# Performance work log

Measured on AMD Instinct MI355X. Metric: run time of the kernel, lower is better.

The kernel has to match this reference:

```python
import jax, jax.numpy as jnp
import numpy as np

MUL0, MUL1 = 64, 32          # 64x0e + 32x1e irreps_emb
D_FEAT = MUL0 + 3 * MUL1     # 160
N_T, N_Q, N_K = 64, 1024, 1024


def quat_apply(q, v):
    # q: (...,4) real-first (w,x,y,z); v: (...,3). Rotate v by q.
    w = q[..., :1]
    u = q[..., 1:]
    uv = jnp.cross(u, v)
    return v + 2.0 * (w * uv + jnp.cross(u, uv))


def split_irreps(f):
    # f: (..., 160) -> scalars (...,64), vectors (...,32,3)
    s = f[..., :MUL0]
    v = f[..., MUL0:].reshape(f.shape[:-1] + (MUL1, 3))
    return s, v


def dtp(a, b, Ws, Wv):
    # Depthwise tensor product restricted to l<=1 (SeparableFCTP analogue),
    # output irreps 1x0e + 32x1e, with SiLU activation on the scalar part.
    sa, va = split_irreps(a)
    sb, vb = split_irreps(b)
    # scalar paths: 0e*0e and 1e.1e (dot) -> 96 scalar channels
    scal = jnp.concatenate([sa * sb, jnp.einsum('...ci,...ci->...c', va, vb)], axis=-1)
    # vector paths: 0e*1e, 1e*0e, 1e x 1e (cross) -> 96 vector channels
    vec = jnp.concatenate(
        [sa[..., :MUL1, None] * vb, va * sb[..., :MUL1, None], jnp.cross(va, vb)], axis=-2)
    out_s = jax.nn.silu(scal @ Ws)                    # (...,1)
    out_v = jnp.einsum('...ci,co->...oi', vec, Wv)    # (...,32,3)
    return out_s, out_v


def get_key_features(points, key_coord, key_feat, W_key):
    # radius-style key lookup: nearest key node + smooth radial envelope + linear
    d2 = jnp.sum((points[:, None, :] - key_coord[None, :, :]) ** 2, axis=-1)  # (M, N_K)
    idx = jnp.argmin(d2, axis=-1)
    dist = jnp.sqrt(jnp.take_along_axis(d2, idx[:, None], axis=1)[:, 0])
    env = jnp.exp(-dist)[:, None]
    return (key_feat[idx] * env) @ W_key              # (M, 160)


def setup_inputs() -> dict:
    key = jax.random.key(0)
    ks = jax.random.split(key, 11)
    return {
        'T': jax.random.normal(ks[0], (N_T, 7), jnp.float32),
        'query_weight': jax.random.uniform(ks[1], (N_Q,), jnp.float32),
        'query_feature': jax.random.normal(ks[2], (N_Q, D_FEAT), jnp.float32),
        'query_coord': jax.random.normal(ks[3], (N_Q, 3), jnp.float32),
        'key_coord': jax.random.normal(ks[4], (N_K, 3), jnp.float32),
        'key_node_feature': jax.random.normal(ks[5], (N_K, D_FEAT), jnp.float32),
        'W_key': jax.random.normal(ks[6], (D_FEAT, D_FEAT), jnp.float32) / np.sqrt(D_FEAT),
        'Ws_lin': jax.random.normal(ks[7], (96, 1), jnp.float32) / np.sqrt(96.0),
        'Wv_lin': jax.random.normal(ks[8], (96, 32), jnp.float32) / np.sqrt(96.0),
        'Ws_ang': jax.random.normal(ks[9], (96, 1), jnp.float32) / np.sqrt(96.0),
        'Wv_ang': jax.random.normal(ks[10], (96, 32), jnp.float32) / np.sqrt(96.0),
    }


def reference(T, query_weight, query_feature, query_coord, key_coord,
              key_node_feature, W_key, Ws_lin, Wv_lin, Ws_ang, Wv_ang):
    n_t = T.shape[0]
    n_q = query_feature.shape[0]
    q = T[:, :4]
    q = q / jnp.linalg.norm(q, axis=-1, keepdims=True)
    X = T[:, 4:]
    # transform query coords by each pose: (N_T, N_Q, 3)
    qc_t = quat_apply(q[:, None, :], query_coord[None, :, :]) + X[:, None, :]
    # equivariant feature transform: scalars unchanged, vectors rotated
    s, v = split_irreps(query_feature)
    v_t = quat_apply(q[:, None, None, :], v[None])                    # (N_T,N_Q,32,3)
    qf_t = jnp.concatenate(
        [jnp.broadcast_to(s, (n_t,) + s.shape), v_t.reshape(n_t, n_q, 3 * MUL1)],
        axis=-1).reshape(n_t * n_q, D_FEAT)
    # key feature gather over the expanded N_T*N_Q batch
    kf = get_key_features(qc_t.reshape(-1, 3), key_coord, key_node_feature, W_key)
    # two tensor products; original drops leading scalar ([..., 1:])
    _, lin = dtp(qf_t, kf, Ws_lin, Wv_lin)
    _, ang = dtp(qf_t, kf, Ws_ang, Wv_ang)
    lin = lin.reshape(n_t, n_q, MUL1, 3).mean(axis=-2)
    ang = ang.reshape(n_t, n_q, MUL1, 3).mean(axis=-2)
    # rotate back into body frame
    qinv = q * jnp.array([1.0, -1.0, -1.0, -1.0], q.dtype)
    lin = quat_apply(qinv[:, None, :], lin)
    ang = quat_apply(qinv[:, None, :], ang)
    ang_orbital = jnp.cross(query_coord[None], lin)
    lin_vel = jnp.einsum('q,tqi->ti', query_weight, lin)
    ang_vel = jnp.einsum('q,tqi->ti', query_weight, ang_orbital + ang)
    return lin_vel, ang_vel
```

## Files before the change

kernel.cpp:

```cpp
#include <hip/hip_runtime.h>
#include <math.h>

#define NT 64
#define NQ 1024
#define NK 1024
#define WS_KW 0
#define WS_QF 131072
#define WS_WV 262144
#define WS_KP 262400

__launch_bounds__(256)
__global__ void prep_kernel(const float* __restrict__ qfeat,
                            const float* __restrict__ keyfeat,
                            const float* __restrict__ Wkey,
                            const float* __restrict__ WvL,
                            const float* __restrict__ WvA,
                            const float* __restrict__ kcoord,
                            float* __restrict__ ws,
                            float* __restrict__ out) {
  const int blk = blockIdx.x;
  const int tid = threadIdx.x;
  if (blk < 128) {
    const int g = blk * 256 + tid;
    const int r = g >> 5;
    const int c = g & 31;
    const float* kf = keyfeat + r * 160;
    const int c0 = 64 + 3 * c;
    float a0 = 0.f, a1 = 0.f, a2 = 0.f, a3 = 0.f;
#pragma unroll 4
    for (int k = 0; k < 160; ++k) {
      const float f = kf[k];
      const float* wr = Wkey + k * 160;
      a0 = fmaf(f, wr[c0 + 0], a0);
      a1 = fmaf(f, wr[c0 + 1], a1);
      a2 = fmaf(f, wr[c0 + 2], a2);
      a3 = fmaf(f, wr[c], a3);
    }
    reinterpret_cast<float4*>(ws + WS_KW)[g] = make_float4(a0, a1, a2, a3);
  } else if (blk < 256) {
    const int g = (blk - 128) * 256 + tid;
    const int p = g >> 5;
    const int c = g & 31;
    const float* q = qfeat + p * 160;
    float4 o = make_float4(q[64 + 3 * c], q[65 + 3 * c], q[66 + 3 * c], q[c]);
    reinterpret_cast<float4*>(ws + WS_QF)[c * 1024 + p] = o;
  } else {
    out[tid] = 0.f;
    if (tid < 128) out[256 + tid] = 0.f;
    float4* kp = reinterpret_cast<float4*>(ws + WS_KP);
#pragma unroll
    for (int j = 0; j < 4; ++j) {
      const int k = j * 256 + tid;
      kp[k] = make_float4(kcoord[k * 3 + 0], kcoord[k * 3 + 1], kcoord[k * 3 + 2], 0.f);
    }
    if (tid < 32) {
      const int c = tid;
      float m0 = 0.f, m1 = 0.f, m2 = 0.f, m3 = 0.f, m4 = 0.f, m5 = 0.f;
      for (int o = 0; o < 32; ++o) {
        m0 += WvL[c * 32 + o];
        m1 += WvL[(32 + c) * 32 + o];
        m2 += WvL[(64 + c) * 32 + o];
        m3 += WvA[c * 32 + o];
        m4 += WvA[(32 + c) * 32 + o];
        m5 += WvA[(64 + c) * 32 + o];
      }
      float* wv = ws + WS_WV + c * 8;
      const float s = 1.0f / 32.0f;
      wv[0] = m0 * s; wv[1] = m1 * s; wv[2] = m2 * s;
      wv[3] = m3 * s; wv[4] = m4 * s; wv[5] = m5 * s;
      wv[6] = 0.f; wv[7] = 0.f;
    }
  }
}

__launch_bounds__(512)
__global__ void main_kernel(const float* __restrict__ T,
                            const float* __restrict__ qweight,
                            const float* __restrict__ qcoord,
                            const float* __restrict__ ws,
                            float* __restrict__ out) {
  __shared__ float4 keys[1024];
  __shared__ float2 cand[8][256];
  __shared__ float red[8][8];
  const int tid  = threadIdx.x;
  const int lane = tid & 63;
  const int wu   = __builtin_amdgcn_readfirstlane(tid >> 6);
  const int t    = blockIdx.x >> 2;
  const int pg   = blockIdx.x & 3;

  {
    const float4* kp = reinterpret_cast<const float4*>(ws + WS_KP);
    keys[tid]       = kp[tid];
    keys[512 + tid] = kp[512 + tid];
  }

  const float* Tt = T + t * 7;
  float qw = Tt[0], qx = Tt[1], qy = Tt[2], qz = Tt[3];
  const float Xx = Tt[4], Xy = Tt[5], Xz = Tt[6];
  const float rn = rsqrtf(qw * qw + qx * qx + qy * qy + qz * qz);
  qw *= rn; qx *= rn; qy *= rn; qz *= rn;
  const float ix = -qx, iy = -qy, iz = -qz;

  float qcx[4], qcy[4], qcz[4];
#pragma unroll
  for (int j = 0; j < 4; ++j) {
    const int q = pg * 256 + j * 64 + lane;
    const float px = qcoord[q * 3 + 0];
    const float py = qcoord[q * 3 + 1];
    const float pz = qcoord[q * 3 + 2];
    const float ux = qy * pz - qz * py;
    const float uy = qz * px - qx * pz;
    const float uz = qx * py - qy * px;
    qcx[j] = px + 2.0f * (qw * ux + (qy * uz - qz * uy)) + Xx;
    qcy[j] = py + 2.0f * (qw * uy + (qz * ux - qx * uz)) + Xy;
    qcz[j] = pz + 2.0f * (qw * uz + (qx * uy - qy * ux)) + Xz;
  }

  __syncthreads();

  const int kbase = wu * 128;
  float mv0 = 1e30f, mv1 = 1e30f, mv2 = 1e30f, mv3 = 1e30f;
  int mi0 = 0, mi1 = 0, mi2 = 0, mi3 = 0;
#pragma unroll 4
  for (int m = 0; m < 128; ++m) {
    const float4 K = keys[kbase + m];
    const float d0x = qcx[0] - K.x, d0y = qcy[0] - K.y, d0z = qcz[0] - K.z;
    const float d1x = qcx[1] - K.x, d1y = qcy[1] - K.y, d1z = qcz[1] - K.z;
    const float d2x = qcx[2] - K.x, d2y = qcy[2] - K.y, d2z = qcz[2] - K.z;
    const float d3x = qcx[3] - K.x, d3y = qcy[3] - K.y, d3z = qcz[3] - K.z;
    const float d0 = d0x * d0x + d0y * d0y + d0z * d0z;
    const float d1 = d1x * d1x + d1y * d1y + d1z * d1z;
    const float d2 = d2x * d2x + d2y * d2y + d2z * d2z;
    const float d3 = d3x * d3x + d3y * d3y + d3z * d3z;
    const int ki = kbase + m;
    if (d0 < mv0) { mv0 = d0; mi0 = ki; }
    if (d1 < mv1) { mv1 = d1; mi1 = ki; }
    if (d2 < mv2) { mv2 = d2; mi2 = ki; }
    if (d3 < mv3) { mv3 = d3; mi3 = ki; }
  }
  cand[wu][0 * 64 + lane] = make_float2(mv0, __int_as_float(mi0));
  cand[wu][1 * 64 + lane] = make_float2(mv1, __int_as_float(mi1));
  cand[wu][2 * 64 + lane] = make_float2(mv2, __int_as_float(mi2));
  cand[wu][3 * 64 + lane] = make_float2(mv3, __int_as_float(mi3));
  __syncthreads();

  const int pl  = tid >> 1;
  const int sub = tid & 1;
  float mv; int mi;
  {
    const float2 c0 = cand[4 * sub][pl];
    mv = c0.x; mi = __float_as_int(c0.y);
#pragma unroll
    for (int i = 1; i < 4; ++i) {
      const float2 ci = cand[4 * sub + i][pl];
      const float vi = ci.x; const int ii = __float_as_int(ci.y);
      if (vi < mv || (vi == mv && ii < mi)) { mv = vi; mi = ii; }
    }
    const float vo = __shfl_xor(mv, 1);
    const int   io = __shfl_xor(mi, 1);
    if (vo < mv || (vo == mv && io < mi)) { mv = vo; mi = io; }
  }
  const int minidx = mi;
  const float env = expf(-sqrtf(mv));

  const int pF = pg * 256 + pl;
  const float qpx = qcoord[pF * 3 + 0];
  const float qpy = qcoord[pF * 3 + 1];
  const float qpz = qcoord[pF * 3 + 2];

  const float4* kwrow = reinterpret_cast<const float4*>(ws + WS_KW) + minidx * 32;
  const float4* qfp   = reinterpret_cast<const float4*>(ws + WS_QF) + pF;
  const float* wv = ws + WS_WV;
  float lx = 0.f, ly = 0.f, lz = 0.f, ax = 0.f, ay = 0.f, az = 0.f;
#pragma unroll
  for (int jj = 0; jj < 16; ++jj) {
    const int c = 2 * jj + sub;
    const float4 B = kwrow[c];
    const float4 A = qfp[c * 1024];
    const float uvx = iy * B.z - iz * B.y;
    const float uvy = iz * B.x - ix * B.z;
    const float uvz = ix * B.y - iy * B.x;
    const float bx = B.x + 2.0f * (qw * uvx + (iy * uvz - iz * uvy));
    const float by = B.y + 2.0f * (qw * uvy + (iz * uvx - ix * uvz));
    const float bz = B.z + 2.0f * (qw * uvz + (ix * uvy - iy * uvx));
    const float crx = A.y * bz - A.z * by;
    const float cry = A.z * bx - A.x * bz;
    const float crz = A.x * by - A.y * bx;
    const float* w6 = wv + c * 8;
    const float a1L = w6[0] * A.w, a2L = w6[1] * B.w, w3L = w6[2];
    const float a1A = w6[3] * A.w, a2A = w6[4] * B.w, w3A = w6[5];
    lx = fmaf(a1L, bx, fmaf(a2L, A.x, fmaf(w3L, crx, lx)));
    ly = fmaf(a1L, by, fmaf(a2L, A.y, fmaf(w3L, cry, ly)));
    lz = fmaf(a1L, bz, fmaf(a2L, A.z, fmaf(w3L, crz, lz)));
    ax = fmaf(a1A, bx, fmaf(a2A, A.x, fmaf(w3A, crx, ax)));
    ay = fmaf(a1A, by, fmaf(a2A, A.y, fmaf(w3A, cry, ay)));
    az = fmaf(a1A, bz, fmaf(a2A, A.z, fmaf(w3A, crz, az)));
  }
  lx += __shfl_xor(lx, 1); ly += __shfl_xor(ly, 1); lz += __shfl_xor(lz, 1);
  ax += __shfl_xor(ax, 1); ay += __shfl_xor(ay, 1); az += __shfl_xor(az, 1);
  lx *= env; ly *= env; lz *= env;
  ax *= env; ay *= env; az *= env;

  const float wp = qweight[pF];
  const float ox = qpy * lz - qpz * ly;
  const float oy = qpz * lx - qpx * lz;
  const float oz = qpx * ly - qpy * lx;
  float r0 = wp * lx, r1 = wp * ly, r2 = wp * lz;
  float r3 = wp * (ox + ax), r4 = wp * (oy + ay), r5 = wp * (oz + az);

#pragma unroll
  for (int m = 32; m >= 1; m >>= 1) {
    r0 += __shfl_xor(r0, m);
    r1 += __shfl_xor(r1, m);
    r2 += __shfl_xor(r2, m);
    r3 += __shfl_xor(r3, m);
    r4 += __shfl_xor(r4, m);
    r5 += __shfl_xor(r5, m);
  }
  if (lane == 0) {
    red[wu][0] = r0; red[wu][1] = r1; red[wu][2] = r2;
    red[wu][3] = r3; red[wu][4] = r4; red[wu][5] = r5;
  }
  __syncthreads();
  if (tid < 6) {
    float s = 0.f;
#pragma unroll
    for (int w = 0; w < 8; ++w) s += red[w][tid];
    const int row = (tid < 3) ? (t * 3 + tid) : (192 + t * 3 + (tid - 3));
    atomicAdd(out + row, s * 0.5f);
  }
}

extern "C" void kernel_launch(void* const* d_in, const int* in_sizes, int n_in,
                              void* d_out, int out_size, void* d_ws, size_t ws_size,
                              hipStream_t stream) {
  const float* T   = (const float*)d_in[0];
  const float* qw  = (const float*)d_in[1];
  const float* qf  = (const float*)d_in[2];
  const float* qc  = (const float*)d_in[3];
  const float* kc  = (const float*)d_in[4];
  const float* kf  = (const float*)d_in[5];
  const float* Wk  = (const float*)d_in[6];
  const float* WvL = (const float*)d_in[8];
  const float* WvA = (const float*)d_in[10];
  float* out = (float*)d_out;
  float* ws  = (float*)d_ws;

  prep_kernel<<<257, 256, 0, stream>>>(qf, kf, Wk, WvL, WvA, kc, ws, out);
  main_kernel<<<256, 512, 0, stream>>>(T, qw, qc, ws, out);
}
```

Before: 109.1 us.

## Repartition main kernel into 1024 blocks with 16-lane key split and shuffle argmin

The main kernel now launches 1024 blocks of 256 threads, each handling 64 queries for one transform. Each query's nearest-key search is split across 16 lanes with interleaved key indices, and the partial argmins are merged by xor-shuffles instead of a cross-wave shared-memory candidate reduction. The feature contraction now splits 4 ways per query instead of 2. This gives more blocks to fill the GPU's compute units and makes the argmin reduction cheaper. In exchange, every block reloads the full 1024-key table into LDS (four times as many blocks doing it) and issues four times as many output atomics.

New measurement: 108.8 us. Within noise of the previous version (-0.3%).

```diff
diff --git a/kernel.cpp b/kernel.cpp
--- a/kernel.cpp
+++ b/kernel.cpp
@@ -73,25 +73,26 @@
   }
 }
 
-__launch_bounds__(512)
+__launch_bounds__(256)
 __global__ void main_kernel(const float* __restrict__ T,
                             const float* __restrict__ qweight,
                             const float* __restrict__ qcoord,
                             const float* __restrict__ ws,
                             float* __restrict__ out) {
   __shared__ float4 keys[1024];
-  __shared__ float2 cand[8][256];
-  __shared__ float red[8][8];
+  __shared__ float2 cand[64];
+  __shared__ float red[4][8];
   const int tid  = threadIdx.x;
   const int lane = tid & 63;
-  const int wu   = __builtin_amdgcn_readfirstlane(tid >> 6);
-  const int t    = blockIdx.x >> 2;
-  const int pg   = blockIdx.x & 3;
+  const int t    = blockIdx.x >> 4;
+  const int qg   = blockIdx.x & 15;
+  const int sub  = tid & 15;
+  const int pl   = tid >> 4;
 
   {
     const float4* kp = reinterpret_cast<const float4*>(ws + WS_KP);
-    keys[tid]       = kp[tid];
-    keys[512 + tid] = kp[512 + tid];
+#pragma unroll
+    for (int j = 0; j < 4; ++j) keys[j * 256 + tid] = kp[j * 256 + tid];
   }
 
   const float* Tt = T + t * 7;
@@ -104,7 +105,7 @@
   float qcx[4], qcy[4], qcz[4];
 #pragma unroll
   for (int j = 0; j < 4; ++j) {
-    const int q = pg * 256 + j * 64 + lane;
+    const int q = qg * 64 + pl * 4 + j;
     const float px = qcoord[q * 3 + 0];
     const float py = qcoord[q * 3 + 1];
     const float pz = qcoord[q * 3 + 2];
@@ -118,12 +119,12 @@
 
   __syncthreads();
 
-  const int kbase = wu * 128;
   float mv0 = 1e30f, mv1 = 1e30f, mv2 = 1e30f, mv3 = 1e30f;
   int mi0 = 0, mi1 = 0, mi2 = 0, mi3 = 0;
-#pragma unroll 4
-  for (int m = 0; m < 128; ++m) {
-    const float4 K = keys[kbase + m];
+#pragma unroll 8
+  for (int m = 0; m < 64; ++m) {
+    const float4 K = keys[16 * m + sub];
+    const int ki = 16 * m + sub;
     const float d0x = qcx[0] - K.x, d0y = qcy[0] - K.y, d0z = qcz[0] - K.z;
     const float d1x = qcx[1] - K.x, d1y = qcy[1] - K.y, d1z = qcz[1] - K.z;
     const float d2x = qcx[2] - K.x, d2y = qcy[2] - K.y, d2z = qcz[2] - K.z;
@@ -132,38 +133,38 @@
     const float d1 = d1x * d1x + d1y * d1y + d1z * d1z;
     const float d2 = d2x * d2x + d2y * d2y + d2z * d2z;
     const float d3 = d3x * d3x + d3y * d3y + d3z * d3z;
-    const int ki = kbase + m;
     if (d0 < mv0) { mv0 = d0; mi0 = ki; }
     if (d1 < mv1) { mv1 = d1; mi1 = ki; }
     if (d2 < mv2) { mv2 = d2; mi2 = ki; }
     if (d3 < mv3) { mv3 = d3; mi3 = ki; }
   }
-  cand[wu][0 * 64 + lane] = make_float2(mv0, __int_as_float(mi0));
-  cand[wu][1 * 64 + lane] = make_float2(mv1, __int_as_float(mi1));
-  cand[wu][2 * 64 + lane] = make_float2(mv2, __int_as_float(mi2));
-  cand[wu][3 * 64 + lane] = make_float2(mv3, __int_as_float(mi3));
+#pragma unroll
+  for (int msk = 1; msk <= 8; msk <<= 1) {
+    float vo; int io;
+    vo = __shfl_xor(mv0, msk); io = __shfl_xor(mi0, msk);
+    if (vo < mv0 || (vo == mv0 && io < mi0)) { mv0 = vo; mi0 = io; }
+    vo = __shfl_xor(mv1, msk); io = __shfl_xor(mi1, msk);
+    if (vo < mv1 || (vo == mv1 && io < mi1)) { mv1 = vo; mi1 = io; }
+    vo = __shfl_xor(mv2, msk); io = __shfl_xor(mi2, msk);
+    if (vo < mv2 || (vo == mv2 && io < mi2)) { mv2 = vo; mi2 = io; }
+    vo = __shfl_xor(mv3, msk); io = __shfl_xor(mi3, msk);
+    if (vo < mv3 || (vo == mv3 && io < mi3)) { mv3 = vo; mi3 = io; }
+  }
+  if (sub == 0) {
+    cand[pl * 4 + 0] = make_float2(mv0, __int_as_float(mi0));
+    cand[pl * 4 + 1] = make_float2(mv1, __int_as_float(mi1));
+    cand[pl * 4 + 2] = make_float2(mv2, __int_as_float(mi2));
+    cand[pl * 4 + 3] = make_float2(mv3, __int_as_float(mi3));
+  }
   __syncthreads();
 
-  const int pl  = tid >> 1;
-  const int sub = tid & 1;
-  float mv; int mi;
-  {
-    const float2 c0 = cand[4 * sub][pl];
-    mv = c0.x; mi = __float_as_int(c0.y);
-#pragma unroll
-    for (int i = 1; i < 4; ++i) {
-      const float2 ci = cand[4 * sub + i][pl];
-      const float vi = ci.x; const int ii = __float_as_int(ci.y);
-      if (vi < mv || (vi == mv && ii < mi)) { mv = vi; mi = ii; }
-    }
-    const float vo = __shfl_xor(mv, 1);
-    const int   io = __shfl_xor(mi, 1);
-    if (vo < mv || (vo == mv && io < mi)) { mv = vo; mi = io; }
-  }
-  const int minidx = mi;
-  const float env = expf(-sqrtf(mv));
-
-  const int pF = pg * 256 + pl;
+  const int pq   = tid >> 2;
+  const int sub2 = tid & 3;
+  const float2 cc = cand[pq];
+  const int minidx = __float_as_int(cc.y);
+  const float env = expf(-sqrtf(cc.x));
+
+  const int pF = qg * 64 + pq;
   const float qpx = qcoord[pF * 3 + 0];
   const float qpy = qcoord[pF * 3 + 1];
   const float qpz = qcoord[pF * 3 + 2];
@@ -173,8 +174,8 @@
   const float* wv = ws + WS_WV;
   float lx = 0.f, ly = 0.f, lz = 0.f, ax = 0.f, ay = 0.f, az = 0.f;
 #pragma unroll
-  for (int jj = 0; jj < 16; ++jj) {
-    const int c = 2 * jj + sub;
+  for (int jj = 0; jj < 8; ++jj) {
+    const int c = 4 * jj + sub2;
     const float4 B = kwrow[c];
     const float4 A = qfp[c * 1024];
     const float uvx = iy * B.z - iz * B.y;
@@ -196,8 +197,11 @@
     ay = fmaf(a1A, by, fmaf(a2A, A.y, fmaf(w3A, cry, ay)));
     az = fmaf(a1A, bz, fmaf(a2A, A.z, fmaf(w3A, crz, az)));
   }
-  lx += __shfl_xor(lx, 1); ly += __shfl_xor(ly, 1); lz += __shfl_xor(lz, 1);
-  ax += __shfl_xor(ax, 1); ay += __shfl_xor(ay, 1); az += __shfl_xor(az, 1);
+#pragma unroll
+  for (int msk = 1; msk <= 2; msk <<= 1) {
+    lx += __shfl_xor(lx, msk); ly += __shfl_xor(ly, msk); lz += __shfl_xor(lz, msk);
+    ax += __shfl_xor(ax, msk); ay += __shfl_xor(ay, msk); az += __shfl_xor(az, msk);
+  }
   lx *= env; ly *= env; lz *= env;
   ax *= env; ay *= env; az *= env;
 
@@ -217,17 +221,16 @@
     r4 += __shfl_xor(r4, m);
     r5 += __shfl_xor(r5, m);
   }
+  const int wave = tid >> 6;
   if (lane == 0) {
-    red[wu][0] = r0; red[wu][1] = r1; red[wu][2] = r2;
-    red[wu][3] = r3; red[wu][4] = r4; red[wu][5] = r5;
+    red[wave][0] = r0; red[wave][1] = r1; red[wave][2] = r2;
+    red[wave][3] = r3; red[wave][4] = r4; red[wave][5] = r5;
   }
   __syncthreads();
   if (tid < 6) {
-    float s = 0.f;
-#pragma unroll
-    for (int w = 0; w < 8; ++w) s += red[w][tid];
+    const float s = red[0][tid] + red[1][tid] + red[2][tid] + red[3][tid];
     const int row = (tid < 3) ? (t * 3 + tid) : (192 + t * 3 + (tid - 3));
-    atomicAdd(out + row, s * 0.5f);
+    atomicAdd(out + row, s * 0.25f);
   }
 }
 
@@ -247,5 +250,5 @@
   float* ws  = (float*)d_ws;
 
   prep_kernel<<<257, 256, 0, stream>>>(qf, kf, Wk, WvL, WvA, kc, ws, out);
-  main_kernel<<<256, 512, 0, stream>>>(T, qw, qc, ws, out);
+  main_kernel<<<1024, 256, 0, stream>>>(T, qw, qc, ws, out);
 }
```
